# Kernel tuning notes

Hardware: AMD Instinct MI355X
Metric: run time of the kernel (lower is better)

## Reference

```python
import jax, jax.numpy as jnp
import numpy as np

H = 128  # hidden width of the PINN MLP


def _mlp_scalar(pt, W0, b0, W1, b1, W2, b2, W3, b3):
    # pt: [2] -> scalar u(x, y); tanh MLP as used in PINN solid-mechanics nets
    h = jnp.tanh(pt @ W0 + b0)
    h = jnp.tanh(h @ W1 + b1)
    h = jnp.tanh(h @ W2 + b2)
    return (h @ W3 + b3)[0]


def setup_inputs() -> dict:
    key = jax.random.key(0)
    ks = jax.random.split(key, 6)
    N = 131072
    # Xavier-ish scaling so tanh stays in its smooth regime
    X = jax.random.normal(ks[0], (N, 2), dtype=jnp.float32)
    W0 = jax.random.normal(ks[1], (2, H), dtype=jnp.float32) * (1.0 / np.sqrt(2.0))
    b0 = jnp.zeros((H,), dtype=jnp.float32)
    W1 = jax.random.normal(ks[2], (H, H), dtype=jnp.float32) * (1.0 / np.sqrt(H))
    b1 = jnp.zeros((H,), dtype=jnp.float32)
    W2 = jax.random.normal(ks[3], (H, H), dtype=jnp.float32) * (1.0 / np.sqrt(H))
    b2 = jnp.zeros((H,), dtype=jnp.float32)
    W3 = jax.random.normal(ks[4], (H, 1), dtype=jnp.float32) * (1.0 / np.sqrt(H))
    b3 = jnp.zeros((1,), dtype=jnp.float32)
    return {"X": X, "W0": W0, "b0": b0, "W1": W1, "b1": b1,
            "W2": W2, "b2": b2, "W3": W3, "b3": b3}


def reference(X, W0, b0, W1, b1, W2, b2, W3, b3):
    # Per-point Hessian of u w.r.t. (x, y). Each collocation point is
    # independent, so TF's batched gradient-of-sum equals the per-point
    # derivative; forward-over-reverse (jacfwd o jacrev) vmapped over N is
    # the efficient fused form of the two nested GradientTapes.
    f = lambda pt: _mlp_scalar(pt, W0, b0, W1, b1, W2, b2, W3, b3)
    hess = jax.vmap(jax.jacfwd(jax.jacrev(f)))(X)  # [N, 2, 2]
    du_dxx = hess[:, 0, 0][:, None]  # [N, 1]
    du_dxy = hess[:, 0, 1][:, None]  # [N, 1]
    du_dyy = hess[:, 1, 1][:, None]  # [N, 1]
    return (du_dxx, du_dxy, du_dyy)
```

## Files before the change

kernel.cpp:

```cpp
#include <hip/hip_runtime.h>

#define H   128
#define P   16
#define NT  256

typedef _Float16 v8h __attribute__((ext_vector_type(8)));
typedef __fp16   h2  __attribute__((ext_vector_type(2)));
typedef float    v4f __attribute__((ext_vector_type(4)));
typedef float    v2f __attribute__((ext_vector_type(2)));

union PK4 { h2 h[4]; uint4 u; };
union PK2 { h2 h[2]; uint2 u; };

__device__ __forceinline__ int soct(int pl, int p, int o) {
    return ((pl * P + p) * 16 + (o ^ (p & 15))) << 3;
}

__global__ void wt_convert(const float* __restrict__ W1,
                           const float* __restrict__ W2,
                           _Float16* __restrict__ ws) {
    const int t = blockIdx.x * 64 + threadIdx.x;
    const int l = t >> 13;
    const int r = t & 8191;
    const int oct = r >> 9;
    const int rem = r & 511;
    const int j  = rem >> 2;
    const int wp = rem & 3;
    const int k  = oct * 8 + 2 * wp;
    const float* __restrict__ W = l ? W2 : W1;
    const float a = W[k * H + j];
    const float b = W[(k + 1) * H + j];
    union { h2 h; unsigned u; } q;
    q.h = __builtin_amdgcn_cvt_pkrtz(a, b);
    ((unsigned*)ws)[t] = q.u;
}

__device__ __forceinline__ v2f tanh_d2_p(v2f z, v2f& g1, v2f& g2) {
    v2f r;
    r.x = __builtin_amdgcn_rcpf(__expf(2.f * z.x) + 1.f);
    r.y = __builtin_amdgcn_rcpf(__expf(2.f * z.y) + 1.f);
    const v2f a = -2.f * r + 1.f;
    g1 = 1.f - a * a;
    g2 = -2.f * (a * g1);
    return a;
}

__global__ __launch_bounds__(NT, 4)
void pinn_hess_mfma(const float* __restrict__ X,
                    const float* __restrict__ W0, const float* __restrict__ b0,
                    const _Float16* __restrict__ Wt,
                    const float* __restrict__ b1, const float* __restrict__ b2,
                    const float* __restrict__ W3,
                    float* __restrict__ out, int N)
{
    __shared__ _Float16 sS[6 * P * H];

    const int tid   = threadIdx.x;
    const int jquad = tid >> 6;
    const int lane  = tid & 63;
    const int quad  = lane >> 4;
    const int l15   = lane & 15;
    const int pbase = blockIdx.x * P;
    const int pmy   = l15;

    {
        const int p = tid >> 4, o = tid & 15;
        const float x = X[2 * (pbase + p)];
        const float y = X[2 * (pbase + p) + 1];
        float wxv[8], wyv[8], bv[8];
        *(float4*)&wxv[0] = *(const float4*)&W0[o * 8];
        *(float4*)&wxv[4] = *(const float4*)&W0[o * 8 + 4];
        *(float4*)&wyv[0] = *(const float4*)&W0[H + o * 8];
        *(float4*)&wyv[4] = *(const float4*)&W0[H + o * 8 + 4];
        *(float4*)&bv[0]  = *(const float4*)&b0[o * 8];
        *(float4*)&bv[4]  = *(const float4*)&b0[o * 8 + 4];
        PK4 q[6];
        #pragma unroll
        for (int hp = 0; hp < 4; ++hp) {
            const v2f wx = {wxv[2*hp], wxv[2*hp+1]};
            const v2f wy = {wyv[2*hp], wyv[2*hp+1]};
            const v2f bb = {bv[2*hp],  bv[2*hp+1]};
            v2f g1, g2;
            const v2f a = tanh_d2_p(x * wx + y * wy + bb, g1, g2);
            const v2f gx = g2 * wx;
            const v2f r0 = a,        r1 = g1 * wx,  r2 = g1 * wy;
            const v2f r3 = gx * wx,  r4 = gx * wy,  r5 = (g2 * wy) * wy;
            q[0].h[hp] = __builtin_amdgcn_cvt_pkrtz(r0.x, r0.y);
            q[1].h[hp] = __builtin_amdgcn_cvt_pkrtz(r1.x, r1.y);
            q[2].h[hp] = __builtin_amdgcn_cvt_pkrtz(r2.x, r2.y);
            q[3].h[hp] = __builtin_amdgcn_cvt_pkrtz(r3.x, r3.y);
            q[4].h[hp] = __builtin_amdgcn_cvt_pkrtz(r4.x, r4.y);
            q[5].h[hp] = __builtin_amdgcn_cvt_pkrtz(r5.x, r5.y);
        }
        #pragma unroll
        for (int pl = 0; pl < 6; ++pl)
            *(uint4*)&sS[soct(pl, p, o)] = q[pl].u;
    }

    const int aoff = quad * H + jquad * 32 + l15;

    for (int layer = 0; layer < 2; ++layer) {
        const v8h* __restrict__ Ag = (const v8h*)(Wt + layer * (16 * H * 8));

        v8h Aa0 = Ag[aoff];
        v8h Aa1 = Ag[aoff + 16];

        __syncthreads();
        __builtin_amdgcn_sched_barrier(0);

        v4f C[6][2];
        #pragma unroll
        for (int pl = 0; pl < 6; ++pl) { C[pl][0] = (v4f){0,0,0,0}; C[pl][1] = (v4f){0,0,0,0}; }

        auto kstep = [&](const v8h A0, const v8h A1, const int kc) {
            const int oct = kc * 4 + quad;
            #pragma unroll
            for (int pl = 0; pl < 6; ++pl) {
                const v8h B = *(const v8h*)&sS[soct(pl, pmy, oct)];
                C[pl][0] = __builtin_amdgcn_mfma_f32_16x16x32_f16(A0, B, C[pl][0], 0, 0, 0);
                C[pl][1] = __builtin_amdgcn_mfma_f32_16x16x32_f16(A1, B, C[pl][1], 0, 0, 0);
            }
        };

        v8h Ab0 = Ag[aoff + 4 * H];
        v8h Ab1 = Ag[aoff + 4 * H + 16];
        kstep(Aa0, Aa1, 0);
        __builtin_amdgcn_sched_barrier(0);

        Aa0 = Ag[aoff + 8 * H];
        Aa1 = Ag[aoff + 8 * H + 16];
        kstep(Ab0, Ab1, 1);
        __builtin_amdgcn_sched_barrier(0);

        Ab0 = Ag[aoff + 12 * H];
        Ab1 = Ag[aoff + 12 * H + 16];
        kstep(Aa0, Aa1, 2);
        __builtin_amdgcn_sched_barrier(0);

        kstep(Ab0, Ab1, 3);

        __syncthreads();

        if (layer == 0) {
            #pragma unroll
            for (int mt = 0; mt < 2; ++mt) {
                const int j0 = jquad * 32 + mt * 16 + quad * 4;
                const float4 bv = *(const float4*)&b1[j0];
                PK2 q[6];
                #pragma unroll
                for (int hp = 0; hp < 2; ++hp) {
                    const v2f zb = hp ? (v2f){C[0][mt][2], C[0][mt][3]}
                                      : (v2f){C[0][mt][0], C[0][mt][1]};
                    const v2f bb = hp ? (v2f){bv.z, bv.w} : (v2f){bv.x, bv.y};
                    const v2f tx = hp ? (v2f){C[1][mt][2], C[1][mt][3]}
                                      : (v2f){C[1][mt][0], C[1][mt][1]};
                    const v2f ty = hp ? (v2f){C[2][mt][2], C[2][mt][3]}
                                      : (v2f){C[2][mt][0], C[2][mt][1]};
                    const v2f cx = hp ? (v2f){C[3][mt][2], C[3][mt][3]}
                                      : (v2f){C[3][mt][0], C[3][mt][1]};
                    const v2f cm = hp ? (v2f){C[4][mt][2], C[4][mt][3]}
                                      : (v2f){C[4][mt][0], C[4][mt][1]};
                    const v2f cy = hp ? (v2f){C[5][mt][2], C[5][mt][3]}
                                      : (v2f){C[5][mt][0], C[5][mt][1]};
                    v2f g1, g2;
                    const v2f a  = tanh_d2_p(zb + bb, g1, g2);
                    const v2f gx = g2 * tx;
                    const v2f s0 = a,        s1 = g1 * tx,          s2 = g1 * ty;
                    const v2f s3 = gx * tx + g1 * cx;
                    const v2f s4 = gx * ty + g1 * cm;
                    const v2f s5 = (g2 * ty) * ty + g1 * cy;
                    q[0].h[hp] = __builtin_amdgcn_cvt_pkrtz(s0.x, s0.y);
                    q[1].h[hp] = __builtin_amdgcn_cvt_pkrtz(s1.x, s1.y);
                    q[2].h[hp] = __builtin_amdgcn_cvt_pkrtz(s2.x, s2.y);
                    q[3].h[hp] = __builtin_amdgcn_cvt_pkrtz(s3.x, s3.y);
                    q[4].h[hp] = __builtin_amdgcn_cvt_pkrtz(s4.x, s4.y);
                    q[5].h[hp] = __builtin_amdgcn_cvt_pkrtz(s5.x, s5.y);
                }
                const int ob = j0 >> 3;
                const int ho = (quad & 1) * 4;
                #pragma unroll
                for (int pl = 0; pl < 6; ++pl)
                    *(uint2*)&sS[soct(pl, pmy, ob) + ho] = q[pl].u;
            }
        } else {
            v2f axx = {0.f, 0.f}, axy = {0.f, 0.f}, ayy = {0.f, 0.f};
            #pragma unroll
            for (int mt = 0; mt < 2; ++mt) {
                const int j0 = jquad * 32 + mt * 16 + quad * 4;
                const float4 bv = *(const float4*)&b2[j0];
                const float4 wv = *(const float4*)&W3[j0];
                #pragma unroll
                for (int hp = 0; hp < 2; ++hp) {
                    const v2f zb = hp ? (v2f){C[0][mt][2], C[0][mt][3]}
                                      : (v2f){C[0][mt][0], C[0][mt][1]};
                    const v2f bb = hp ? (v2f){bv.z, bv.w} : (v2f){bv.x, bv.y};
                    const v2f w3 = hp ? (v2f){wv.z, wv.w} : (v2f){wv.x, wv.y};
                    const v2f tx = hp ? (v2f){C[1][mt][2], C[1][mt][3]}
                                      : (v2f){C[1][mt][0], C[1][mt][1]};
                    const v2f ty = hp ? (v2f){C[2][mt][2], C[2][mt][3]}
                                      : (v2f){C[2][mt][0], C[2][mt][1]};
                    const v2f cx = hp ? (v2f){C[3][mt][2], C[3][mt][3]}
                                      : (v2f){C[3][mt][0], C[3][mt][1]};
                    const v2f cm = hp ? (v2f){C[4][mt][2], C[4][mt][3]}
                                      : (v2f){C[4][mt][0], C[4][mt][1]};
                    const v2f cy = hp ? (v2f){C[5][mt][2], C[5][mt][3]}
                                      : (v2f){C[5][mt][0], C[5][mt][1]};
                    v2f g1, g2;
                    tanh_d2_p(zb + bb, g1, g2);
                    const v2f gx = g2 * tx;
                    axx = axx + w3 * (gx * tx + g1 * cx);
                    axy = axy + w3 * (gx * ty + g1 * cm);
                    ayy = ayy + w3 * ((g2 * ty) * ty + g1 * cy);
                }
            }
            float oxx = axx.x + axx.y, oxy = axy.x + axy.y, oyy = ayy.x + ayy.y;
            oxx += __shfl_xor(oxx, 16); oxx += __shfl_xor(oxx, 32);
            oxy += __shfl_xor(oxy, 16); oxy += __shfl_xor(oxy, 32);
            oyy += __shfl_xor(oyy, 16); oyy += __shfl_xor(oyy, 32);
            float* sRed = (float*)sS;
            if (quad == 0) {
                sRed[0 * 64 + jquad * 16 + pmy] = oxx;
                sRed[1 * 64 + jquad * 16 + pmy] = oxy;
                sRed[2 * 64 + jquad * 16 + pmy] = oyy;
            }
            __syncthreads();
            if (tid < 48) {
                const int c = tid >> 4, p = tid & 15;
                float acc = 0.f;
                #pragma unroll
                for (int jq = 0; jq < 4; ++jq)
                    acc += sRed[c * 64 + jq * 16 + p];
                out[c * N + pbase + p] = acc;
            }
        }
    }
}

extern "C" void kernel_launch(void* const* d_in, const int* in_sizes, int n_in,
                              void* d_out, int out_size, void* d_ws, size_t ws_size,
                              hipStream_t stream) {
    const float* X  = (const float*)d_in[0];
    const float* W0 = (const float*)d_in[1];
    const float* b0 = (const float*)d_in[2];
    const float* W1 = (const float*)d_in[3];
    const float* b1 = (const float*)d_in[4];
    const float* W2 = (const float*)d_in[5];
    const float* b2 = (const float*)d_in[6];
    const float* W3 = (const float*)d_in[7];

    const int N = in_sizes[0] / 2;
    float* out = (float*)d_out;
    _Float16* ws = (_Float16*)d_ws;

    hipLaunchKernelGGL(wt_convert, dim3(256), dim3(64), 0, stream, W1, W2, ws);

    hipLaunchKernelGGL(pinn_hess_mfma, dim3(N / P), dim3(NT), 0, stream,
                       X, W0, b0, ws, b1, b2, W3, out, N);
}
```

Before: 138.9 us.

## Ping-pong two point groups per block to overlap MFMA and tanh epilogue

Doubles the block to 512 threads with two 256-thread groups, each owning its own shared-memory tile and 16 points. The stages are staggered by one step so one group runs MFMA GEMMs while the other runs the tanh/derivative epilogue or layer-0 setup, separated by block-wide barriers. The aim is to overlap matrix-core work with VALU/transcendental work inside a CU. In exchange it uses twice the LDS per block, adds extra barriers, and launch_bounds (NT,4) now implies 2048 threads per CU, which may squeeze register allocation or occupancy.

```diff
diff --git a/kernel.cpp b/kernel.cpp
--- a/kernel.cpp
+++ b/kernel.cpp
@@ -2,7 +2,7 @@
 
 #define H   128
 #define P   16
-#define NT  256
+#define NT  512
 
 typedef _Float16 v8h __attribute__((ext_vector_type(8)));
 typedef __fp16   h2  __attribute__((ext_vector_type(2)));
@@ -53,18 +53,25 @@
                     const float* __restrict__ W3,
                     float* __restrict__ out, int N)
 {
-    __shared__ _Float16 sS[6 * P * H];
+    __shared__ _Float16 sS[2 * 6 * P * H];
 
     const int tid   = threadIdx.x;
-    const int jquad = tid >> 6;
+    const int grp   = tid >> 8;
+    const int tl    = tid & 255;
+    const int jquad = (tid >> 6) & 3;
     const int lane  = tid & 63;
     const int quad  = lane >> 4;
     const int l15   = lane & 15;
-    const int pbase = blockIdx.x * P;
+    const int pbase = blockIdx.x * (2 * P) + grp * P;
     const int pmy   = l15;
-
-    {
-        const int p = tid >> 4, o = tid & 15;
+    _Float16* sSg   = &sS[grp * (6 * P * H)];
+
+    const int aoff = quad * H + jquad * 32 + l15;
+
+    v4f C[6][2];
+
+    auto L0 = [&]() {
+        const int p = tl >> 4, o = tl & 15;
         const float x = X[2 * (pbase + p)];
         const float y = X[2 * (pbase + p) + 1];
         float wxv[8], wyv[8], bv[8];
@@ -94,146 +101,150 @@
         }
         #pragma unroll
         for (int pl = 0; pl < 6; ++pl)
-            *(uint4*)&sS[soct(pl, p, o)] = q[pl].u;
-    }
-
-    const int aoff = quad * H + jquad * 32 + l15;
-
-    for (int layer = 0; layer < 2; ++layer) {
+            *(uint4*)&sSg[soct(pl, p, o)] = q[pl].u;
+    };
+
+    auto GEMM = [&](int layer) {
         const v8h* __restrict__ Ag = (const v8h*)(Wt + layer * (16 * H * 8));
-
+        #pragma unroll
+        for (int pl = 0; pl < 6; ++pl) { C[pl][0] = (v4f){0,0,0,0}; C[pl][1] = (v4f){0,0,0,0}; }
         v8h Aa0 = Ag[aoff];
         v8h Aa1 = Ag[aoff + 16];
-
-        __syncthreads();
-        __builtin_amdgcn_sched_barrier(0);
-
-        v4f C[6][2];
-        #pragma unroll
-        for (int pl = 0; pl < 6; ++pl) { C[pl][0] = (v4f){0,0,0,0}; C[pl][1] = (v4f){0,0,0,0}; }
-
+        v8h Ab0 = Ag[aoff + 4 * H];
+        v8h Ab1 = Ag[aoff + 4 * H + 16];
         auto kstep = [&](const v8h A0, const v8h A1, const int kc) {
             const int oct = kc * 4 + quad;
             #pragma unroll
             for (int pl = 0; pl < 6; ++pl) {
-                const v8h B = *(const v8h*)&sS[soct(pl, pmy, oct)];
+                const v8h B = *(const v8h*)&sSg[soct(pl, pmy, oct)];
                 C[pl][0] = __builtin_amdgcn_mfma_f32_16x16x32_f16(A0, B, C[pl][0], 0, 0, 0);
                 C[pl][1] = __builtin_amdgcn_mfma_f32_16x16x32_f16(A1, B, C[pl][1], 0, 0, 0);
             }
         };
-
-        v8h Ab0 = Ag[aoff + 4 * H];
-        v8h Ab1 = Ag[aoff + 4 * H + 16];
         kstep(Aa0, Aa1, 0);
         __builtin_amdgcn_sched_barrier(0);
-
         Aa0 = Ag[aoff + 8 * H];
         Aa1 = Ag[aoff + 8 * H + 16];
         kstep(Ab0, Ab1, 1);
         __builtin_amdgcn_sched_barrier(0);
-
         Ab0 = Ag[aoff + 12 * H];
         Ab1 = Ag[aoff + 12 * H + 16];
         kstep(Aa0, Aa1, 2);
         __builtin_amdgcn_sched_barrier(0);
-
         kstep(Ab0, Ab1, 3);
-
-        __syncthreads();
-
-        if (layer == 0) {
-            #pragma unroll
-            for (int mt = 0; mt < 2; ++mt) {
-                const int j0 = jquad * 32 + mt * 16 + quad * 4;
-                const float4 bv = *(const float4*)&b1[j0];
-                PK2 q[6];
-                #pragma unroll
-                for (int hp = 0; hp < 2; ++hp) {
-                    const v2f zb = hp ? (v2f){C[0][mt][2], C[0][mt][3]}
-                                      : (v2f){C[0][mt][0], C[0][mt][1]};
-                    const v2f bb = hp ? (v2f){bv.z, bv.w} : (v2f){bv.x, bv.y};
-                    const v2f tx = hp ? (v2f){C[1][mt][2], C[1][mt][3]}
-                                      : (v2f){C[1][mt][0], C[1][mt][1]};
-                    const v2f ty = hp ? (v2f){C[2][mt][2], C[2][mt][3]}
-                                      : (v2f){C[2][mt][0], C[2][mt][1]};
-                    const v2f cx = hp ? (v2f){C[3][mt][2], C[3][mt][3]}
-                                      : (v2f){C[3][mt][0], C[3][mt][1]};
-                    const v2f cm = hp ? (v2f){C[4][mt][2], C[4][mt][3]}
-                                      : (v2f){C[4][mt][0], C[4][mt][1]};
-                    const v2f cy = hp ? (v2f){C[5][mt][2], C[5][mt][3]}
-                                      : (v2f){C[5][mt][0], C[5][mt][1]};
-                    v2f g1, g2;
-                    const v2f a  = tanh_d2_p(zb + bb, g1, g2);
-                    const v2f gx = g2 * tx;
-                    const v2f s0 = a,        s1 = g1 * tx,          s2 = g1 * ty;
-                    const v2f s3 = gx * tx + g1 * cx;
-                    const v2f s4 = gx * ty + g1 * cm;
-                    const v2f s5 = (g2 * ty) * ty + g1 * cy;
-                    q[0].h[hp] = __builtin_amdgcn_cvt_pkrtz(s0.x, s0.y);
-                    q[1].h[hp] = __builtin_amdgcn_cvt_pkrtz(s1.x, s1.y);
-                    q[2].h[hp] = __builtin_amdgcn_cvt_pkrtz(s2.x, s2.y);
-                    q[3].h[hp] = __builtin_amdgcn_cvt_pkrtz(s3.x, s3.y);
-                    q[4].h[hp] = __builtin_amdgcn_cvt_pkrtz(s4.x, s4.y);
-                    q[5].h[hp] = __builtin_amdgcn_cvt_pkrtz(s5.x, s5.y);
-                }
-                const int ob = j0 >> 3;
-                const int ho = (quad & 1) * 4;
-                #pragma unroll
-                for (int pl = 0; pl < 6; ++pl)
-                    *(uint2*)&sS[soct(pl, pmy, ob) + ho] = q[pl].u;
+    };
+
+    auto E1 = [&]() {
+        #pragma unroll
+        for (int mt = 0; mt < 2; ++mt) {
+            const int j0 = jquad * 32 + mt * 16 + quad * 4;
+            const float4 bv = *(const float4*)&b1[j0];
+            PK2 q[6];
+            #pragma unroll
+            for (int hp = 0; hp < 2; ++hp) {
+                const v2f zb = hp ? (v2f){C[0][mt][2], C[0][mt][3]}
+                                  : (v2f){C[0][mt][0], C[0][mt][1]};
+                const v2f bb = hp ? (v2f){bv.z, bv.w} : (v2f){bv.x, bv.y};
+                const v2f tx = hp ? (v2f){C[1][mt][2], C[1][mt][3]}
+                                  : (v2f){C[1][mt][0], C[1][mt][1]};
+                const v2f ty = hp ? (v2f){C[2][mt][2], C[2][mt][3]}
+                                  : (v2f){C[2][mt][0], C[2][mt][1]};
+                const v2f cx = hp ? (v2f){C[3][mt][2], C[3][mt][3]}
+                                  : (v2f){C[3][mt][0], C[3][mt][1]};
+                const v2f cm = hp ? (v2f){C[4][mt][2], C[4][mt][3]}
+                                  : (v2f){C[4][mt][0], C[4][mt][1]};
+                const v2f cy = hp ? (v2f){C[5][mt][2], C[5][mt][3]}
+                                  : (v2f){C[5][mt][0], C[5][mt][1]};
+                v2f g1, g2;
+                const v2f a  = tanh_d2_p(zb + bb, g1, g2);
+                const v2f gx = g2 * tx;
+                const v2f s0 = a,        s1 = g1 * tx,          s2 = g1 * ty;
+                const v2f s3 = gx * tx + g1 * cx;
+                const v2f s4 = gx * ty + g1 * cm;
+                const v2f s5 = (g2 * ty) * ty + g1 * cy;
+                q[0].h[hp] = __builtin_amdgcn_cvt_pkrtz(s0.x, s0.y);
+                q[1].h[hp] = __builtin_amdgcn_cvt_pkrtz(s1.x, s1.y);
+                q[2].h[hp] = __builtin_amdgcn_cvt_pkrtz(s2.x, s2.y);
+                q[3].h[hp] = __builtin_amdgcn_cvt_pkrtz(s3.x, s3.y);
+                q[4].h[hp] = __builtin_amdgcn_cvt_pkrtz(s4.x, s4.y);
+                q[5].h[hp] = __builtin_amdgcn_cvt_pkrtz(s5.x, s5.y);
             }
-        } else {
-            v2f axx = {0.f, 0.f}, axy = {0.f, 0.f}, ayy = {0.f, 0.f};
-            #pragma unroll
-            for (int mt = 0; mt < 2; ++mt) {
-                const int j0 = jquad * 32 + mt * 16 + quad * 4;
-                const float4 bv = *(const float4*)&b2[j0];
-                const float4 wv = *(const float4*)&W3[j0];
-                #pragma unroll
-                for (int hp = 0; hp < 2; ++hp) {
-                    const v2f zb = hp ? (v2f){C[0][mt][2], C[0][mt][3]}
-                                      : (v2f){C[0][mt][0], C[0][mt][1]};
-                    const v2f bb = hp ? (v2f){bv.z, bv.w} : (v2f){bv.x, bv.y};
-                    const v2f w3 = hp ? (v2f){wv.z, wv.w} : (v2f){wv.x, wv.y};
-                    const v2f tx = hp ? (v2f){C[1][mt][2], C[1][mt][3]}
-                                      : (v2f){C[1][mt][0], C[1][mt][1]};
-                    const v2f ty = hp ? (v2f){C[2][mt][2], C[2][mt][3]}
-                                      : (v2f){C[2][mt][0], C[2][mt][1]};
-                    const v2f cx = hp ? (v2f){C[3][mt][2], C[3][mt][3]}
-                                      : (v2f){C[3][mt][0], C[3][mt][1]};
-                    const v2f cm = hp ? (v2f){C[4][mt][2], C[4][mt][3]}
-                                      : (v2f){C[4][mt][0], C[4][mt][1]};
-                    const v2f cy = hp ? (v2f){C[5][mt][2], C[5][mt][3]}
-                                      : (v2f){C[5][mt][0], C[5][mt][1]};
-                    v2f g1, g2;
-                    tanh_d2_p(zb + bb, g1, g2);
-                    const v2f gx = g2 * tx;
-                    axx = axx + w3 * (gx * tx + g1 * cx);
-                    axy = axy + w3 * (gx * ty + g1 * cm);
-                    ayy = ayy + w3 * ((g2 * ty) * ty + g1 * cy);
-                }
+            const int ob = j0 >> 3;
+            const int ho = (quad & 1) * 4;
+            #pragma unroll
+            for (int pl = 0; pl < 6; ++pl)
+                *(uint2*)&sSg[soct(pl, pmy, ob) + ho] = q[pl].u;
+        }
+    };
+
+    auto E2a = [&]() {
+        v2f axx = {0.f, 0.f}, axy = {0.f, 0.f}, ayy = {0.f, 0.f};
+        #pragma unroll
+        for (int mt = 0; mt < 2; ++mt) {
+            const int j0 = jquad * 32 + mt * 16 + quad * 4;
+            const float4 bv = *(const float4*)&b2[j0];
+            const float4 wv = *(const float4*)&W3[j0];
+            #pragma unroll
+            for (int hp = 0; hp < 2; ++hp) {
+                const v2f zb = hp ? (v2f){C[0][mt][2], C[0][mt][3]}
+                                  : (v2f){C[0][mt][0], C[0][mt][1]};
+                const v2f bb = hp ? (v2f){bv.z, bv.w} : (v2f){bv.x, bv.y};
+                const v2f w3 = hp ? (v2f){wv.z, wv.w} : (v2f){wv.x, wv.y};
+                const v2f tx = hp ? (v2f){C[1][mt][2], C[1][mt][3]}
+                                  : (v2f){C[1][mt][0], C[1][mt][1]};
+                const v2f ty = hp ? (v2f){C[2][mt][2], C[2][mt][3]}
+                                  : (v2f){C[2][mt][0], C[2][mt][1]};
+                const v2f cx = hp ? (v2f){C[3][mt][2], C[3][mt][3]}
+                                  : (v2f){C[3][mt][0], C[3][mt][1]};
+                const v2f cm = hp ? (v2f){C[4][mt][2], C[4][mt][3]}
+                                  : (v2f){C[4][mt][0], C[4][mt][1]};
+                const v2f cy = hp ? (v2f){C[5][mt][2], C[5][mt][3]}
+                                  : (v2f){C[5][mt][0], C[5][mt][1]};
+                v2f g1, g2;
+                tanh_d2_p(zb + bb, g1, g2);
+                const v2f gx = g2 * tx;
+                axx = axx + w3 * (gx * tx + g1 * cx);
+                axy = axy + w3 * (gx * ty + g1 * cm);
+                ayy = ayy + w3 * ((g2 * ty) * ty + g1 * cy);
             }
-            float oxx = axx.x + axx.y, oxy = axy.x + axy.y, oyy = ayy.x + ayy.y;
-            oxx += __shfl_xor(oxx, 16); oxx += __shfl_xor(oxx, 32);
-            oxy += __shfl_xor(oxy, 16); oxy += __shfl_xor(oxy, 32);
-            oyy += __shfl_xor(oyy, 16); oyy += __shfl_xor(oyy, 32);
-            float* sRed = (float*)sS;
-            if (quad == 0) {
-                sRed[0 * 64 + jquad * 16 + pmy] = oxx;
-                sRed[1 * 64 + jquad * 16 + pmy] = oxy;
-                sRed[2 * 64 + jquad * 16 + pmy] = oyy;
-            }
-            __syncthreads();
-            if (tid < 48) {
-                const int c = tid >> 4, p = tid & 15;
-                float acc = 0.f;
-                #pragma unroll
-                for (int jq = 0; jq < 4; ++jq)
-                    acc += sRed[c * 64 + jq * 16 + p];
-                out[c * N + pbase + p] = acc;
-            }
-        }
-    }
+        }
+        float oxx = axx.x + axx.y, oxy = axy.x + axy.y, oyy = ayy.x + ayy.y;
+        oxx += __shfl_xor(oxx, 16); oxx += __shfl_xor(oxx, 32);
+        oxy += __shfl_xor(oxy, 16); oxy += __shfl_xor(oxy, 32);
+        oyy += __shfl_xor(oyy, 16); oyy += __shfl_xor(oyy, 32);
+        float* sRed = (float*)sSg;
+        if (quad == 0) {
+            sRed[0 * 64 + jquad * 16 + pmy] = oxx;
+            sRed[1 * 64 + jquad * 16 + pmy] = oxy;
+            sRed[2 * 64 + jquad * 16 + pmy] = oyy;
+        }
+    };
+
+    auto E2b = [&]() {
+        float* sRed = (float*)sSg;
+        if (tl < 48) {
+            const int c = tl >> 4, p = tl & 15;
+            float acc = 0.f;
+            #pragma unroll
+            for (int jq = 0; jq < 4; ++jq)
+                acc += sRed[c * 64 + jq * 16 + p];
+            out[c * N + pbase + p] = acc;
+        }
+    };
+
+    if (grp == 0) L0();
+    __syncthreads();
+    if (grp == 0) GEMM(0); else L0();
+    __syncthreads();
+    if (grp == 0) E1();    else GEMM(0);
+    __syncthreads();
+    if (grp == 0) GEMM(1); else E1();
+    __syncthreads();
+    if (grp == 0) E2a();   else GEMM(1);
+    __syncthreads();
+    if (grp == 0) E2b();   else E2a();
+    __syncthreads();
+    if (grp == 1) E2b();
 }
 
 extern "C" void kernel_launch(void* const* d_in, const int* in_sizes, int n_in,
@@ -254,6 +265,6 @@
 
     hipLaunchKernelGGL(wt_convert, dim3(256), dim3(64), 0, stream, W1, W2, ws);
 
-    hipLaunchKernelGGL(pinn_hess_mfma, dim3(N / P), dim3(NT), 0, stream,
+    hipLaunchKernelGGL(pinn_hess_mfma, dim3(N / (2 * P)), dim3(NT), 0, stream,
                        X, W0, b0, ws, b1, b2, W3, out, N);
 }
```

Measured after the change: 139.5 us. About the same (+0.4%).

## Split hidden dimension across eight waves per block instead of four

Applied to the files above, without the earlier changes.

Doubles the block to 512 threads so each of eight waves owns 16 output columns instead of 32. Each wave now issues half the MFMAs per k-step against the same shared B tiles, and the manual A-prefetch double buffering and sched barriers are removed in favour of a simple unrolled loop. The aim is more waves in flight per CU to hide latency, at the cost of each B fragment being read from LDS by twice as many waves and a larger cross-wave reduction.

```diff
diff --git a/kernel.cpp b/kernel.cpp
--- a/kernel.cpp
+++ b/kernel.cpp
@@ -2,14 +2,13 @@
 
 #define H   128
 #define P   16
-#define NT  256
+#define NT  512
 
 typedef _Float16 v8h __attribute__((ext_vector_type(8)));
 typedef __fp16   h2  __attribute__((ext_vector_type(2)));
 typedef float    v4f __attribute__((ext_vector_type(4)));
 typedef float    v2f __attribute__((ext_vector_type(2)));
 
-union PK4 { h2 h[4]; uint4 u; };
 union PK2 { h2 h[2]; uint2 u; };
 
 __device__ __forceinline__ int soct(int pl, int p, int o) {
@@ -45,7 +44,7 @@
     return a;
 }
 
-__global__ __launch_bounds__(NT, 4)
+__global__ __launch_bounds__(NT, 8)
 void pinn_hess_mfma(const float* __restrict__ X,
                     const float* __restrict__ W0, const float* __restrict__ b0,
                     const _Float16* __restrict__ Wt,
@@ -64,22 +63,18 @@
     const int pmy   = l15;
 
     {
-        const int p = tid >> 4, o = tid & 15;
+        const int p = tid >> 5, q4 = tid & 31;
         const float x = X[2 * (pbase + p)];
         const float y = X[2 * (pbase + p) + 1];
-        float wxv[8], wyv[8], bv[8];
-        *(float4*)&wxv[0] = *(const float4*)&W0[o * 8];
-        *(float4*)&wxv[4] = *(const float4*)&W0[o * 8 + 4];
-        *(float4*)&wyv[0] = *(const float4*)&W0[H + o * 8];
-        *(float4*)&wyv[4] = *(const float4*)&W0[H + o * 8 + 4];
-        *(float4*)&bv[0]  = *(const float4*)&b0[o * 8];
-        *(float4*)&bv[4]  = *(const float4*)&b0[o * 8 + 4];
-        PK4 q[6];
-        #pragma unroll
-        for (int hp = 0; hp < 4; ++hp) {
-            const v2f wx = {wxv[2*hp], wxv[2*hp+1]};
-            const v2f wy = {wyv[2*hp], wyv[2*hp+1]};
-            const v2f bb = {bv[2*hp],  bv[2*hp+1]};
+        const float4 wx4 = *(const float4*)&W0[q4 * 4];
+        const float4 wy4 = *(const float4*)&W0[H + q4 * 4];
+        const float4 bb4 = *(const float4*)&b0[q4 * 4];
+        PK2 q[6];
+        #pragma unroll
+        for (int hp = 0; hp < 2; ++hp) {
+            const v2f wx = hp ? (v2f){wx4.z, wx4.w} : (v2f){wx4.x, wx4.y};
+            const v2f wy = hp ? (v2f){wy4.z, wy4.w} : (v2f){wy4.x, wy4.y};
+            const v2f bb = hp ? (v2f){bb4.z, bb4.w} : (v2f){bb4.x, bb4.y};
             v2f g1, g2;
             const v2f a = tanh_d2_p(x * wx + y * wy + bb, g1, g2);
             const v2f gx = g2 * wx;
@@ -92,126 +87,90 @@
             q[4].h[hp] = __builtin_amdgcn_cvt_pkrtz(r4.x, r4.y);
             q[5].h[hp] = __builtin_amdgcn_cvt_pkrtz(r5.x, r5.y);
         }
+        const int o  = q4 >> 1;
+        const int ho = (q4 & 1) * 4;
         #pragma unroll
         for (int pl = 0; pl < 6; ++pl)
-            *(uint4*)&sS[soct(pl, p, o)] = q[pl].u;
+            *(uint2*)&sS[soct(pl, p, o) + ho] = q[pl].u;
     }
 
-    const int aoff = quad * H + jquad * 32 + l15;
+    const int aoff = quad * H + jquad * 16 + l15;
 
     for (int layer = 0; layer < 2; ++layer) {
         const v8h* __restrict__ Ag = (const v8h*)(Wt + layer * (16 * H * 8));
 
-        v8h Aa0 = Ag[aoff];
-        v8h Aa1 = Ag[aoff + 16];
-
         __syncthreads();
-        __builtin_amdgcn_sched_barrier(0);
-
-        v4f C[6][2];
-        #pragma unroll
-        for (int pl = 0; pl < 6; ++pl) { C[pl][0] = (v4f){0,0,0,0}; C[pl][1] = (v4f){0,0,0,0}; }
-
-        auto kstep = [&](const v8h A0, const v8h A1, const int kc) {
+
+        v4f C[6];
+        #pragma unroll
+        for (int pl = 0; pl < 6; ++pl) C[pl] = (v4f){0, 0, 0, 0};
+
+        #pragma unroll
+        for (int kc = 0; kc < 4; ++kc) {
+            const v8h A = Ag[aoff + kc * 4 * H];
             const int oct = kc * 4 + quad;
             #pragma unroll
             for (int pl = 0; pl < 6; ++pl) {
                 const v8h B = *(const v8h*)&sS[soct(pl, pmy, oct)];
-                C[pl][0] = __builtin_amdgcn_mfma_f32_16x16x32_f16(A0, B, C[pl][0], 0, 0, 0);
-                C[pl][1] = __builtin_amdgcn_mfma_f32_16x16x32_f16(A1, B, C[pl][1], 0, 0, 0);
-            }
-        };
-
-        v8h Ab0 = Ag[aoff + 4 * H];
-        v8h Ab1 = Ag[aoff + 4 * H + 16];
-        kstep(Aa0, Aa1, 0);
-        __builtin_amdgcn_sched_barrier(0);
-
-        Aa0 = Ag[aoff + 8 * H];
-        Aa1 = Ag[aoff + 8 * H + 16];
-        kstep(Ab0, Ab1, 1);
-        __builtin_amdgcn_sched_barrier(0);
-
-        Ab0 = Ag[aoff + 12 * H];
-        Ab1 = Ag[aoff + 12 * H + 16];
-        kstep(Aa0, Aa1, 2);
-        __builtin_amdgcn_sched_barrier(0);
-
-        kstep(Ab0, Ab1, 3);
+                C[pl] = __builtin_amdgcn_mfma_f32_16x16x32_f16(A, B, C[pl], 0, 0, 0);
+            }
+        }
 
         __syncthreads();
 
+        const int j0 = jquad * 16 + quad * 4;
+
         if (layer == 0) {
-            #pragma unroll
-            for (int mt = 0; mt < 2; ++mt) {
-                const int j0 = jquad * 32 + mt * 16 + quad * 4;
-                const float4 bv = *(const float4*)&b1[j0];
-                PK2 q[6];
-                #pragma unroll
-                for (int hp = 0; hp < 2; ++hp) {
-                    const v2f zb = hp ? (v2f){C[0][mt][2], C[0][mt][3]}
-                                      : (v2f){C[0][mt][0], C[0][mt][1]};
-                    const v2f bb = hp ? (v2f){bv.z, bv.w} : (v2f){bv.x, bv.y};
-                    const v2f tx = hp ? (v2f){C[1][mt][2], C[1][mt][3]}
-                                      : (v2f){C[1][mt][0], C[1][mt][1]};
-                    const v2f ty = hp ? (v2f){C[2][mt][2], C[2][mt][3]}
-                                      : (v2f){C[2][mt][0], C[2][mt][1]};
-                    const v2f cx = hp ? (v2f){C[3][mt][2], C[3][mt][3]}
-                                      : (v2f){C[3][mt][0], C[3][mt][1]};
-                    const v2f cm = hp ? (v2f){C[4][mt][2], C[4][mt][3]}
-                                      : (v2f){C[4][mt][0], C[4][mt][1]};
-                    const v2f cy = hp ? (v2f){C[5][mt][2], C[5][mt][3]}
-                                      : (v2f){C[5][mt][0], C[5][mt][1]};
-                    v2f g1, g2;
-                    const v2f a  = tanh_d2_p(zb + bb, g1, g2);
-                    const v2f gx = g2 * tx;
-                    const v2f s0 = a,        s1 = g1 * tx,          s2 = g1 * ty;
-                    const v2f s3 = gx * tx + g1 * cx;
-                    const v2f s4 = gx * ty + g1 * cm;
-                    const v2f s5 = (g2 * ty) * ty + g1 * cy;
-                    q[0].h[hp] = __builtin_amdgcn_cvt_pkrtz(s0.x, s0.y);
-                    q[1].h[hp] = __builtin_amdgcn_cvt_pkrtz(s1.x, s1.y);
-                    q[2].h[hp] = __builtin_amdgcn_cvt_pkrtz(s2.x, s2.y);
-                    q[3].h[hp] = __builtin_amdgcn_cvt_pkrtz(s3.x, s3.y);
-                    q[4].h[hp] = __builtin_amdgcn_cvt_pkrtz(s4.x, s4.y);
-                    q[5].h[hp] = __builtin_amdgcn_cvt_pkrtz(s5.x, s5.y);
-                }
-                const int ob = j0 >> 3;
-                const int ho = (quad & 1) * 4;
-                #pragma unroll
-                for (int pl = 0; pl < 6; ++pl)
-                    *(uint2*)&sS[soct(pl, pmy, ob) + ho] = q[pl].u;
-            }
+            const float4 bv = *(const float4*)&b1[j0];
+            PK2 q[6];
+            #pragma unroll
+            for (int hp = 0; hp < 2; ++hp) {
+                const v2f zb = hp ? (v2f){C[0][2], C[0][3]} : (v2f){C[0][0], C[0][1]};
+                const v2f bb = hp ? (v2f){bv.z, bv.w}       : (v2f){bv.x, bv.y};
+                const v2f tx = hp ? (v2f){C[1][2], C[1][3]} : (v2f){C[1][0], C[1][1]};
+                const v2f ty = hp ? (v2f){C[2][2], C[2][3]} : (v2f){C[2][0], C[2][1]};
+                const v2f cx = hp ? (v2f){C[3][2], C[3][3]} : (v2f){C[3][0], C[3][1]};
+                const v2f cm = hp ? (v2f){C[4][2], C[4][3]} : (v2f){C[4][0], C[4][1]};
+                const v2f cy = hp ? (v2f){C[5][2], C[5][3]} : (v2f){C[5][0], C[5][1]};
+                v2f g1, g2;
+                const v2f a  = tanh_d2_p(zb + bb, g1, g2);
+                const v2f gx = g2 * tx;
+                const v2f s0 = a,        s1 = g1 * tx,          s2 = g1 * ty;
+                const v2f s3 = gx * tx + g1 * cx;
+                const v2f s4 = gx * ty + g1 * cm;
+                const v2f s5 = (g2 * ty) * ty + g1 * cy;
+                q[0].h[hp] = __builtin_amdgcn_cvt_pkrtz(s0.x, s0.y);
+                q[1].h[hp] = __builtin_amdgcn_cvt_pkrtz(s1.x, s1.y);
+                q[2].h[hp] = __builtin_amdgcn_cvt_pkrtz(s2.x, s2.y);
+                q[3].h[hp] = __builtin_amdgcn_cvt_pkrtz(s3.x, s3.y);
+                q[4].h[hp] = __builtin_amdgcn_cvt_pkrtz(s4.x, s4.y);
+                q[5].h[hp] = __builtin_amdgcn_cvt_pkrtz(s5.x, s5.y);
+            }
+            const int ob = j0 >> 3;
+            const int ho = (quad & 1) * 4;
+            #pragma unroll
+            for (int pl = 0; pl < 6; ++pl)
+                *(uint2*)&sS[soct(pl, pmy, ob) + ho] = q[pl].u;
         } else {
             v2f axx = {0.f, 0.f}, axy = {0.f, 0.f}, ayy = {0.f, 0.f};
-            #pragma unroll
-            for (int mt = 0; mt < 2; ++mt) {
-                const int j0 = jquad * 32 + mt * 16 + quad * 4;
-                const float4 bv = *(const float4*)&b2[j0];
-                const float4 wv = *(const float4*)&W3[j0];
-                #pragma unroll
-                for (int hp = 0; hp < 2; ++hp) {
-                    const v2f zb = hp ? (v2f){C[0][mt][2], C[0][mt][3]}
-                                      : (v2f){C[0][mt][0], C[0][mt][1]};
-                    const v2f bb = hp ? (v2f){bv.z, bv.w} : (v2f){bv.x, bv.y};
-                    const v2f w3 = hp ? (v2f){wv.z, wv.w} : (v2f){wv.x, wv.y};
-                    const v2f tx = hp ? (v2f){C[1][mt][2], C[1][mt][3]}
-                                      : (v2f){C[1][mt][0], C[1][mt][1]};
-                    const v2f ty = hp ? (v2f){C[2][mt][2], C[2][mt][3]}
-                                      : (v2f){C[2][mt][0], C[2][mt][1]};
-                    const v2f cx = hp ? (v2f){C[3][mt][2], C[3][mt][3]}
-                                      : (v2f){C[3][mt][0], C[3][mt][1]};
-                    const v2f cm = hp ? (v2f){C[4][mt][2], C[4][mt][3]}
-                                      : (v2f){C[4][mt][0], C[4][mt][1]};
-                    const v2f cy = hp ? (v2f){C[5][mt][2], C[5][mt][3]}
-                                      : (v2f){C[5][mt][0], C[5][mt][1]};
-                    v2f g1, g2;
-                    tanh_d2_p(zb + bb, g1, g2);
-                    const v2f gx = g2 * tx;
-                    axx = axx + w3 * (gx * tx + g1 * cx);
-                    axy = axy + w3 * (gx * ty + g1 * cm);
-                    ayy = ayy + w3 * ((g2 * ty) * ty + g1 * cy);
-                }
+            const float4 bv = *(const float4*)&b2[j0];
+            const float4 wv = *(const float4*)&W3[j0];
+            #pragma unroll
+            for (int hp = 0; hp < 2; ++hp) {
+                const v2f zb = hp ? (v2f){C[0][2], C[0][3]} : (v2f){C[0][0], C[0][1]};
+                const v2f bb = hp ? (v2f){bv.z, bv.w}       : (v2f){bv.x, bv.y};
+                const v2f w3 = hp ? (v2f){wv.z, wv.w}       : (v2f){wv.x, wv.y};
+                const v2f tx = hp ? (v2f){C[1][2], C[1][3]} : (v2f){C[1][0], C[1][1]};
+                const v2f ty = hp ? (v2f){C[2][2], C[2][3]} : (v2f){C[2][0], C[2][1]};
+                const v2f cx = hp ? (v2f){C[3][2], C[3][3]} : (v2f){C[3][0], C[3][1]};
+                const v2f cm = hp ? (v2f){C[4][2], C[4][3]} : (v2f){C[4][0], C[4][1]};
+                const v2f cy = hp ? (v2f){C[5][2], C[5][3]} : (v2f){C[5][0], C[5][1]};
+                v2f g1, g2;
+                tanh_d2_p(zb + bb, g1, g2);
+                const v2f gx = g2 * tx;
+                axx = axx + w3 * (gx * tx + g1 * cx);
+                axy = axy + w3 * (gx * ty + g1 * cm);
+                ayy = ayy + w3 * ((g2 * ty) * ty + g1 * cy);
             }
             float oxx = axx.x + axx.y, oxy = axy.x + axy.y, oyy = ayy.x + ayy.y;
             oxx += __shfl_xor(oxx, 16); oxx += __shfl_xor(oxx, 32);
@@ -219,17 +178,17 @@
             oyy += __shfl_xor(oyy, 16); oyy += __shfl_xor(oyy, 32);
             float* sRed = (float*)sS;
             if (quad == 0) {
-                sRed[0 * 64 + jquad * 16 + pmy] = oxx;
-                sRed[1 * 64 + jquad * 16 + pmy] = oxy;
-                sRed[2 * 64 + jquad * 16 + pmy] = oyy;
+                sRed[0 * 128 + jquad * 16 + pmy] = oxx;
+                sRed[1 * 128 + jquad * 16 + pmy] = oxy;
+                sRed[2 * 128 + jquad * 16 + pmy] = oyy;
             }
             __syncthreads();
             if (tid < 48) {
                 const int c = tid >> 4, p = tid & 15;
                 float acc = 0.f;
                 #pragma unroll
-                for (int jq = 0; jq < 4; ++jq)
-                    acc += sRed[c * 64 + jq * 16 + p];
+                for (int jq = 0; jq < 8; ++jq)
+                    acc += sRed[c * 128 + jq * 16 + p];
                 out[c * N + pbase + p] = acc;
             }
         }
```

After: 136.6 us. About the same (-1.6%).
